# Kernel tuning notes

Measured on AMD Instinct MI355X. Metric: run time of the kernel, lower is better.

Reference implementation:

```python
import jax, jax.numpy as jnp
import numpy as np

B, L, D, H, M = 2, 1024, 1024, 16, 64
DH = D // H  # depth per head


def setup_inputs() -> dict:
    key = jax.random.key(0)
    ks = jax.random.split(key, 7)
    s = 0.02
    return {
        "x": jax.random.normal(ks[0], (B, L, D), jnp.float32),
        "Wq": jax.random.normal(ks[1], (D, D), jnp.float32) * s,
        "Wk": jax.random.normal(ks[2], (D, D), jnp.float32) * s,
        "Wv": jax.random.normal(ks[3], (D, D), jnp.float32) * s,
        "Wo": jax.random.normal(ks[4], (D, D), jnp.float32) * s,
        "rel_k_table": jax.random.normal(ks[5], (2 * M + 1, DH), jnp.float32) * s,
        "rel_v_table": jax.random.normal(ks[6], (2 * M + 1, DH), jnp.float32) * s,
    }


def _rel_idx(length, max_rel):
    # Shaw-style clipped relative position indices: [L, L] in [0, 2*max_rel]
    r = jnp.arange(length)
    return jnp.clip(r[None, :] - r[:, None], -max_rel, max_rel) + max_rel


def _split_heads(t):
    # [B, L, D] -> [B, H, L, DH]
    return t.reshape(B, L, H, DH).transpose(0, 2, 1, 3)


def reference(x, Wq, Wk, Wv, Wo, rel_k_table, rel_v_table):
    q = _split_heads(x @ Wq) * (DH ** -0.5)  # T2T scales q by d_head^-0.5
    k = _split_heads(x @ Wk)
    v = _split_heads(x @ Wv)

    idx = _rel_idx(L, M)
    rel_k = rel_k_table[idx]  # [L, L, DH] gathered keys-relative embeddings
    rel_v = rel_v_table[idx]  # [L, L, DH]

    # _relative_attention_inner(q, k, rel_k, transpose=True)
    logits = jnp.einsum('bhid,bhjd->bhij', q, k) + jnp.einsum('bhid,ijd->bhij', q, rel_k)
    w = jax.nn.softmax(logits, axis=-1)  # [B, H, L, L]; dropout_rate=0 / inference

    # _relative_attention_inner(w, v, rel_v, transpose=False)
    o = jnp.einsum('bhij,bhjd->bhid', w, v) + jnp.einsum('bhij,ijd->bhid', w, rel_v)

    # combine heads then output transform
    o = o.transpose(0, 2, 1, 3).reshape(B, L, D)
    return o @ Wo
```

## Files before the change

### kernel.cpp

```cpp
#include <hip/hip_runtime.h>
#include <hip/hip_bf16.h>
#include <math.h>

#define B_ 2
#define L_ 1024
#define D_ 1024
#define H_ 16
#define DH_ 64
#define M_ 64
#define R_ 129
#define NLD ((size_t)B_ * L_ * D_)
#define DD  ((size_t)D_ * D_)
#define QSCALE 0.18033688011112042f

using bf16x8 = __attribute__((ext_vector_type(8))) short;
using f32x4  = __attribute__((ext_vector_type(4))) float;

__device__ __forceinline__ unsigned short f2bf(float f) {
    unsigned int x = __builtin_bit_cast(unsigned int, f);
    unsigned int r = x + 0x7fffu + ((x >> 16) & 1u);
    return (unsigned short)(r >> 16);
}
__device__ __forceinline__ float bf2f(unsigned short u) {
    unsigned int x = ((unsigned int)u) << 16;
    return __builtin_bit_cast(float, x);
}
__device__ __forceinline__ unsigned int pk2bf(float lo, float hi) {
    __hip_bfloat162 h = __float22bfloat162_rn(float2{lo, hi});
    unsigned int u;
    __builtin_memcpy(&u, &h, 4);
    return u;
}

__global__ __launch_bounds__(256)
void prep(const float* __restrict__ x,
          const float* __restrict__ W0, const float* __restrict__ W1,
          const float* __restrict__ W2, const float* __restrict__ W3,
          const float* __restrict__ relk, const float* __restrict__ relv,
          unsigned short* __restrict__ xb, unsigned short* __restrict__ Wt,
          unsigned short* __restrict__ relkb, unsigned short* __restrict__ relvT)
{
    __shared__ float tile[32][33];
    const int bid = blockIdx.x, t = threadIdx.x;
    if (bid < 2048) {
        const int i = bid * 256 + t;
        float4 v = ((const float4*)x)[i];
        short4 o = { (short)f2bf(v.x), (short)f2bf(v.y), (short)f2bf(v.z), (short)f2bf(v.w) };
        ((short4*)xb)[i] = o;
    } else if (bid < 6144) {
        const int wb = bid - 2048;
        const int z = wb >> 10, rem = wb & 1023;
        const float* W = z == 0 ? W0 : z == 1 ? W1 : z == 2 ? W2 : W3;
        unsigned short* T = Wt + (size_t)z * DD;
        const int k0 = (rem >> 5) * 32, n0 = (rem & 31) * 32;
        const int r = t >> 3, c = (t & 7) * 4;
        float4 v = *(const float4*)&W[(size_t)(k0 + r) * D_ + n0 + c];
        tile[r][c] = v.x; tile[r][c + 1] = v.y; tile[r][c + 2] = v.z; tile[r][c + 3] = v.w;
        __syncthreads();
        short4 o = { (short)f2bf(tile[c][r]),     (short)f2bf(tile[c + 1][r]),
                     (short)f2bf(tile[c + 2][r]), (short)f2bf(tile[c + 3][r]) };
        *(short4*)&T[(size_t)(n0 + r) * D_ + k0 + c] = o;
    } else {
        const int idx = (bid - 6144) * 256 + t;
        if (idx < 144 * 64) {
            const int r = idx >> 6, d = idx & 63;
            relkb[idx] = (r < R_) ? f2bf(relk[r * 64 + d]) : (unsigned short)0;
        }
        if (idx < 64 * 136) {
            const int d = idx / 136, r = idx - d * 136;
            relvT[idx] = (r < R_) ? f2bf(relv[r * 64 + d]) : (unsigned short)0;
        }
    }
}

__global__ __launch_bounds__(256)
void gemm64(const unsigned short* __restrict__ A, const unsigned short* __restrict__ Bt,
            unsigned short* __restrict__ Cb, float* __restrict__ Cf, float scale0)
{
    __shared__ unsigned short As[64][64];
    __shared__ unsigned short Bs[128][64];

    const int t = threadIdx.x, lane = t & 63, wid = t >> 6;
    const int fr = lane & 15, g = lane >> 4;
    const int m0 = blockIdx.y * 64;
    const int nglob = blockIdx.x * 128;
    const int mat = nglob >> 10;
    const int n0 = nglob & 1023;
    const float scale = (mat == 0) ? scale0 : 1.f;
    const int wm = (wid >> 1) * 32, wn = (wid & 1) * 64;

    f32x4 acc[2][4] = {};

    int arow[2], akof[2], adst[2];
#pragma unroll
    for (int c = 0; c < 2; ++c) {
        const int chunk = c * 256 + t;
        arow[c] = chunk >> 3;
        akof[c] = ((chunk & 7) ^ (arow[c] & 7)) * 8;
        adst[c] = chunk * 8;
    }
    int brow[4], bkof[4], bdst[4];
#pragma unroll
    for (int c = 0; c < 4; ++c) {
        const int chunk = c * 256 + t;
        brow[c] = chunk >> 3;
        bkof[c] = ((chunk & 7) ^ (brow[c] & 7)) * 8;
        bdst[c] = chunk * 8;
    }

    const unsigned short* Abase = A  + (size_t)m0 * D_;
    const unsigned short* Bbase = Bt + (size_t)nglob * D_;

    for (int k0 = 0; k0 < D_; k0 += 64) {
        __syncthreads();
#pragma unroll
        for (int c = 0; c < 2; ++c)
            __builtin_amdgcn_global_load_lds(
                (const __attribute__((address_space(1))) void*)(Abase + (size_t)arow[c] * D_ + k0 + akof[c]),
                (__attribute__((address_space(3))) void*)(&As[0][0] + adst[c]), 16, 0, 0);
#pragma unroll
        for (int c = 0; c < 4; ++c)
            __builtin_amdgcn_global_load_lds(
                (const __attribute__((address_space(1))) void*)(Bbase + (size_t)brow[c] * D_ + k0 + bkof[c]),
                (__attribute__((address_space(3))) void*)(&Bs[0][0] + bdst[c]), 16, 0, 0);
        __syncthreads();

#pragma unroll
        for (int kb = 0; kb < 2; ++kb) {
            bf16x8 av[2], bv[4];
#pragma unroll
            for (int i = 0; i < 2; ++i) {
                const int ra = wm + i * 16 + fr;
                av[i] = *(const bf16x8*)&As[ra][(((kb << 2) + g) ^ (ra & 7)) * 8];
            }
#pragma unroll
            for (int j = 0; j < 4; ++j) {
                const int rb = wn + j * 16 + fr;
                bv[j] = *(const bf16x8*)&Bs[rb][(((kb << 2) + g) ^ (rb & 7)) * 8];
            }
#pragma unroll
            for (int i = 0; i < 2; ++i)
#pragma unroll
                for (int j = 0; j < 4; ++j)
                    acc[i][j] = __builtin_amdgcn_mfma_f32_16x16x32_bf16(av[i], bv[j], acc[i][j], 0, 0, 0);
        }
    }

    const int orow = g * 4;
    if (Cb) {
        unsigned short* Cp = Cb + (size_t)mat * NLD;
#pragma unroll
        for (int i = 0; i < 2; ++i)
#pragma unroll
            for (int j = 0; j < 4; ++j) {
                unsigned short* cp = Cp + (size_t)(m0 + wm + i * 16 + orow) * D_ + n0 + wn + j * 16 + fr;
#pragma unroll
                for (int rg = 0; rg < 4; ++rg)
                    cp[(size_t)rg * D_] = f2bf(acc[i][j][rg] * scale);
            }
    } else {
#pragma unroll
        for (int i = 0; i < 2; ++i)
#pragma unroll
            for (int j = 0; j < 4; ++j) {
                float* cp = Cf + (size_t)(m0 + wm + i * 16 + orow) * D_ + n0 + wn + j * 16 + fr;
#pragma unroll
                for (int rg = 0; rg < 4; ++rg)
                    cp[(size_t)rg * D_] = acc[i][j][rg] * scale;
            }
    }
}

__device__ __forceinline__ void stage_k(const unsigned short* src, unsigned short* dst, int t)
{
#pragma unroll
    for (int it = 0; it < 2; ++it) {
        const int c = it * 256 + t;
        const int j = c >> 3;
        const int sc = (c & 7) ^ (j & 7);
        __builtin_amdgcn_global_load_lds(
            (const __attribute__((address_space(1))) void*)(src + (size_t)j * D_ + sc * 8),
            (__attribute__((address_space(3))) void*)(dst + c * 8), 16, 0, 0);
    }
}

__device__ __forceinline__ void write_vt(unsigned short (*Vtl)[64], int jp, int d0, bf16x8 a, bf16x8 b)
{
    const int jlo = (2 * jp) & 7;
    const int jc  = jp >> 2;
#pragma unroll
    for (int e = 0; e < 8; ++e) {
        const int d = d0 + e;
        const unsigned int val = (unsigned int)(unsigned short)a[e]
                               | ((unsigned int)(unsigned short)b[e] << 16);
        *(unsigned int*)&Vtl[d][((jc ^ (d & 7)) << 3) + jlo] = val;
    }
}

__global__ __launch_bounds__(256)
void attn_mfma(const unsigned short* __restrict__ Qb, const unsigned short* __restrict__ Kb,
               const unsigned short* __restrict__ Vb,
               const unsigned short* __restrict__ relkb,
               const unsigned short* __restrict__ relvT,
               const float* __restrict__ relv,
               unsigned short* __restrict__ Ob)
{
    __shared__ unsigned short Klds[2][64][64];
    __shared__ unsigned short Vt[64][64];
    __shared__ unsigned short Plds[64][72];
    __shared__ unsigned short QW[64][136];

    const int t    = threadIdx.x;
    const int lane = t & 63;
    const int w    = t >> 6;
    const int fr   = lane & 15;
    const int g    = lane >> 4;

    const int bx  = blockIdx.x;
    const int xcd = bx & 7, slot = bx >> 3;
    const int bh  = (xcd << 2) | (slot >> 4);
    const int rb  = slot & 15;
    const int b   = bh >> 4, h = bh & 15;
    const int i0  = rb * 64;
    const size_t head = (size_t)b * L_ * D_ + (size_t)h * DH_;

    const int iloc = w * 16 + fr;

    const unsigned short* Kh = Kb + head;
    const unsigned short* Vh = Vb + head;

    stage_k(Kh, &Klds[0][0][0], t);

    const int jp = t & 31, d0v = ((t >> 5) & 7) * 8;
    bf16x8 va  = *(const bf16x8*)(Vh + (size_t)(2 * jp) * D_ + d0v);
    bf16x8 vb2 = *(const bf16x8*)(Vh + (size_t)(2 * jp + 1) * D_ + d0v);

    bf16x8 qf[2];
    {
        const unsigned short* qp = Qb + head + (size_t)(i0 + iloc) * D_;
        qf[0] = *(const bf16x8*)(qp + g * 8);
        qf[1] = *(const bf16x8*)(qp + 32 + g * 8);
    }

#pragma unroll
    for (int rc = 0; rc < 9; ++rc) {
        f32x4 acc = {};
#pragma unroll
        for (int kb = 0; kb < 2; ++kb) {
            bf16x8 rv = *(const bf16x8*)&relkb[(size_t)(rc * 16 + fr) * 64 + kb * 32 + g * 8];
            acc = __builtin_amdgcn_mfma_f32_16x16x32_bf16(rv, qf[kb], acc, 0, 0, 0);
        }
        if (rc < 8) {
            uint2 pk = { pk2bf(acc[0], acc[1]), pk2bf(acc[2], acc[3]) };
            *(uint2*)&QW[iloc][rc * 16 + g * 4] = pk;
        } else if (g == 0) {
            QW[iloc][128] = f2bf(acc[0]);
        }
    }
    if (rb == 0) {
        for (int c = 1 + g; c <= 63 - iloc; c += 4) QW[iloc][c] = 0;
    } else if (rb == 15) {
        for (int c = 128 - iloc + g; c <= 127; c += 4) QW[iloc][c] = 0;
    }

    write_vt(Vt, jp, d0v, va, vb2);
    asm volatile("s_waitcnt vmcnt(0)" ::: "memory");
    __syncthreads();

    const float qr0   = bf2f(QW[iloc][0]);
    const float qr128 = bf2f(QW[iloc][128]);

    f32x4 oacc[4] = {};
    float lpart = 0.f, pe0p = 0.f, pe128p = 0.f;

    int bb = 0;
    for (int jt = 0; jt < 16; ++jt) {
        const bool pre = (jt < 15);
        if (pre) {
            stage_k(Kh + (size_t)(jt + 1) * 64 * D_, &Klds[bb ^ 1][0][0], t);
            const unsigned short* vp = Vh + (size_t)((jt + 1) * 64 + 2 * jp) * D_ + d0v;
            va  = *(const bf16x8*)vp;
            vb2 = *(const bf16x8*)(vp + D_);
        }

        f32x4 s[4];
        __builtin_amdgcn_s_setprio(1);
#pragma unroll
        for (int fc = 0; fc < 4; ++fc) {
            f32x4 a = {};
            const int j = fc * 16 + fr;
#pragma unroll
            for (int kb = 0; kb < 2; ++kb) {
                bf16x8 kv = *(const bf16x8*)&Klds[bb][j][(((kb << 2) + g) ^ (j & 7)) * 8];
                a = __builtin_amdgcn_mfma_f32_16x16x32_bf16(kv, qf[kb], a, 0, 0, 0);
            }
            s[fc] = a;
        }
        __builtin_amdgcn_s_setprio(0);

        bf16x8 vv0[4], vv1[4];
#pragma unroll
        for (int fd = 0; fd < 4; ++fd) {
            const int d = fd * 16 + fr;
            vv0[fd] = *(const bf16x8*)&Vt[d][((g)     ^ (d & 7)) * 8];
            vv1[fd] = *(const bf16x8*)&Vt[d][((4 + g) ^ (d & 7)) * 8];
        }

        const int dt   = (jt - rb) * 64;
        const int relb = dt - iloc + g * 4;

        if (dt <= -128 || dt >= 128) {
            const float qrc = (dt < 0) ? qr0 : qr128;
            float tsum = 0.f;
#pragma unroll
            for (int fc = 0; fc < 4; ++fc) {
                float p0 = exp2f(s[fc][0] + qrc);
                float p1 = exp2f(s[fc][1] + qrc);
                float p2 = exp2f(s[fc][2] + qrc);
                float p3 = exp2f(s[fc][3] + qrc);
                uint2 pk = { pk2bf(p0, p1), pk2bf(p2, p3) };
                *(uint2*)&Plds[iloc][fc * 16 + g * 4] = pk;
                tsum += (p0 + p1) + (p2 + p3);
            }
            lpart += tsum;
            if (dt < 0) pe0p += tsum; else pe128p += tsum;
        } else if (dt == 0) {
#pragma unroll
            for (int fc = 0; fc < 4; ++fc) {
                const int c0 = relb + fc * 16 + M_;
                float pe[4];
#pragma unroll
                for (int reg = 0; reg < 4; ++reg) {
                    pe[reg] = exp2f(s[fc][reg] + bf2f(QW[iloc][c0 + reg]));
                    lpart += pe[reg];
                }
                uint2 pk = { pk2bf(pe[0], pe[1]), pk2bf(pe[2], pe[3]) };
                *(uint2*)&Plds[iloc][fc * 16 + g * 4] = pk;
                QW[iloc][c0 + 0] = (unsigned short)(pk.x & 0xffffu);
                QW[iloc][c0 + 1] = (unsigned short)(pk.x >> 16);
                QW[iloc][c0 + 2] = (unsigned short)(pk.y & 0xffffu);
                QW[iloc][c0 + 3] = (unsigned short)(pk.y >> 16);
            }
        } else {
#pragma unroll
            for (int fc = 0; fc < 4; ++fc) {
                float pe[4];
#pragma unroll
                for (int reg = 0; reg < 4; ++reg) {
                    const int colr = relb + fc * 16 + reg + M_;
                    const int col  = colr < 0 ? 0 : (colr > 128 ? 128 : colr);
                    pe[reg] = exp2f(s[fc][reg] + bf2f(QW[iloc][col]));
                    lpart += pe[reg];
                    if (col == 0)        pe0p   += pe[reg];
                    else if (col == 128) pe128p += pe[reg];
                    else                 QW[iloc][col] = f2bf(pe[reg]);
                }
                uint2 pk = { pk2bf(pe[0], pe[1]), pk2bf(pe[2], pe[3]) };
                *(uint2*)&Plds[iloc][fc * 16 + g * 4] = pk;
            }
        }

        asm volatile("s_waitcnt lgkmcnt(0)" ::: "memory");
        __builtin_amdgcn_sched_barrier(0);

        bf16x8 pa0 = *(const bf16x8*)&Plds[iloc][g * 8];
        bf16x8 pa1 = *(const bf16x8*)&Plds[iloc][32 + g * 8];
        __builtin_amdgcn_s_setprio(1);
#pragma unroll
        for (int fd = 0; fd < 4; ++fd) {
            oacc[fd] = __builtin_amdgcn_mfma_f32_16x16x32_bf16(pa0, vv0[fd], oacc[fd], 0, 0, 0);
            oacc[fd] = __builtin_amdgcn_mfma_f32_16x16x32_bf16(pa1, vv1[fd], oacc[fd], 0, 0, 0);
        }
        __builtin_amdgcn_s_setprio(0);

        if (pre) {
            asm volatile("s_waitcnt lgkmcnt(0)" ::: "memory");
            __builtin_amdgcn_s_barrier();
            write_vt(Vt, jp, d0v, va, vb2);
        }
        asm volatile("s_waitcnt vmcnt(0)" ::: "memory");
        __syncthreads();
        bb ^= 1;
    }

    lpart  += __shfl_xor(lpart, 16);  lpart  += __shfl_xor(lpart, 32);
    pe0p   += __shfl_xor(pe0p, 16);   pe0p   += __shfl_xor(pe0p, 32);
    pe128p += __shfl_xor(pe128p, 16); pe128p += __shfl_xor(pe128p, 32);
    if (g == 0) {
        QW[iloc][0]   = f2bf(pe0p);
        QW[iloc][128] = f2bf(pe128p);
    }
    asm volatile("s_waitcnt lgkmcnt(0)" ::: "memory");
    __builtin_amdgcn_sched_barrier(0);

#pragma unroll
    for (int kc = 0; kc < 4; ++kc) {
        bf16x8 wa = *(const bf16x8*)&QW[iloc][kc * 32 + g * 8];
#pragma unroll
        for (int fd = 0; fd < 4; ++fd) {
            bf16x8 rv = *(const bf16x8*)&relvT[(size_t)(fd * 16 + fr) * 136 + kc * 32 + g * 8];
            oacc[fd] = __builtin_amdgcn_mfma_f32_16x16x32_bf16(wa, rv, oacc[fd], 0, 0, 0);
        }
    }

    float invd[4], pr128[4];
#pragma unroll
    for (int reg = 0; reg < 4; ++reg) {
        const int src = (lane & 48) | (g * 4 + reg);
        invd[reg]  = 1.f / __shfl(lpart, src, 64);
        pr128[reg] = __shfl(pe128p, src, 64);
    }

#pragma unroll
    for (int fd = 0; fd < 4; ++fd) {
        const float r128 = relv[128 * 64 + fd * 16 + fr];
        unsigned short* op = Ob + head + (size_t)(i0 + w * 16 + g * 4) * D_ + fd * 16 + fr;
#pragma unroll
        for (int reg = 0; reg < 4; ++reg)
            op[(size_t)reg * D_] = f2bf((oacc[fd][reg] + pr128[reg] * r128) * invd[reg]);
    }
}

extern "C" void kernel_launch(void* const* d_in, const int* in_sizes, int n_in,
                              void* d_out, int out_size, void* d_ws, size_t ws_size,
                              hipStream_t stream)
{
    const float* x    = (const float*)d_in[0];
    const float* Wq   = (const float*)d_in[1];
    const float* Wk   = (const float*)d_in[2];
    const float* Wv   = (const float*)d_in[3];
    const float* Wo   = (const float*)d_in[4];
    const float* relk = (const float*)d_in[5];
    const float* relv = (const float*)d_in[6];
    float* out = (float*)d_out;

    unsigned short* xb    = (unsigned short*)d_ws;
    unsigned short* Wt    = xb + NLD;
    unsigned short* relkb = Wt + 4 * DD;
    unsigned short* relvT = relkb + 144 * 64;
    unsigned short* QKVb  = relvT + 64 * 136;
    unsigned short* Ob    = QKVb + 3 * NLD;

    prep<<<dim3(6180), 256, 0, stream>>>(x, Wq, Wk, Wv, Wo, relk, relv, xb, Wt, relkb, relvT);

    gemm64<<<dim3(24, 32), 256, 0, stream>>>(xb, Wt, QKVb, nullptr, QSCALE);

    attn_mfma<<<dim3(512), 256, 0, stream>>>(QKVb, QKVb + NLD, QKVb + 2 * NLD,
                                             relkb, relvT, relv, Ob);

    gemm64<<<dim3(8, 32), 256, 0, stream>>>(Ob, Wt + 3 * DD, nullptr, out, 1.f);
}
```

Before: 81.70 us.

## Split attention key tiles across wave pairs with 32-row query blocks

The attention kernel now processes 32 query rows per block instead of 64, and the four waves split into two row groups by two key-column halves. Each wave handles 32 of the 64 keys per tile, and partial softmax sums and output accumulators are reduced through shared memory at the end. The grid doubles to 1024 blocks to raise parallelism and occupancy. In exchange, each block stages the same K/V tiles for half as many rows, so K/V global traffic per output doubles, and the end of the kernel gains extra barriers and a cross-wave reduction.

```diff
diff --git a/kernel.cpp b/kernel.cpp
--- a/kernel.cpp
+++ b/kernel.cpp
@@ -207,24 +207,28 @@
 {
     __shared__ unsigned short Klds[2][64][64];
     __shared__ unsigned short Vt[64][64];
-    __shared__ unsigned short Plds[64][72];
-    __shared__ unsigned short QW[64][136];
+    __shared__ unsigned short Plds[32][88];
+    __shared__ unsigned short QW[32][136];
+    __shared__ float lred[2][32], p0red[2][32], p128red[2][32];
 
     const int t    = threadIdx.x;
     const int lane = t & 63;
     const int w    = t >> 6;
     const int fr   = lane & 15;
     const int g    = lane >> 4;
+    const int wr   = w & 1;
+    const int wj   = w >> 1;
 
     const int bx  = blockIdx.x;
     const int xcd = bx & 7, slot = bx >> 3;
-    const int bh  = (xcd << 2) | (slot >> 4);
-    const int rb  = slot & 15;
+    const int bh  = (xcd << 2) | (slot >> 5);
+    const int rb  = slot & 31;
     const int b   = bh >> 4, h = bh & 15;
-    const int i0  = rb * 64;
+    const int i0  = rb * 32;
     const size_t head = (size_t)b * L_ * D_ + (size_t)h * DH_;
 
-    const int iloc = w * 16 + fr;
+    const int iloc = wr * 16 + fr;
+    const int ig   = i0 + iloc;
 
     const unsigned short* Kh = Kb + head;
     const unsigned short* Vh = Vb + head;
@@ -237,13 +241,12 @@
 
     bf16x8 qf[2];
     {
-        const unsigned short* qp = Qb + head + (size_t)(i0 + iloc) * D_;
+        const unsigned short* qp = Qb + head + (size_t)ig * D_;
         qf[0] = *(const bf16x8*)(qp + g * 8);
         qf[1] = *(const bf16x8*)(qp + 32 + g * 8);
     }
 
-#pragma unroll
-    for (int rc = 0; rc < 9; ++rc) {
+    auto qr_block = [&](int rc) {
         f32x4 acc = {};
 #pragma unroll
         for (int kb = 0; kb < 2; ++kb) {
@@ -256,11 +259,18 @@
         } else if (g == 0) {
             QW[iloc][128] = f2bf(acc[0]);
         }
-    }
-    if (rb == 0) {
-        for (int c = 1 + g; c <= 63 - iloc; c += 4) QW[iloc][c] = 0;
-    } else if (rb == 15) {
-        for (int c = 128 - iloc + g; c <= 127; c += 4) QW[iloc][c] = 0;
+    };
+    if (wj == 0) { qr_block(0); qr_block(1); qr_block(2); qr_block(3); qr_block(8); }
+    else         { qr_block(4); qr_block(5); qr_block(6); qr_block(7); }
+
+    {
+        const int lo_end = 63 - ig;
+        const int hi_beg = 1088 - ig;
+        if (wj == 0) {
+            for (int c = 1 + g; c <= lo_end; c += 4) QW[iloc][c] = 0;
+        } else {
+            for (int c = hi_beg + g; c <= 127; c += 4) QW[iloc][c] = 0;
+        }
     }
 
     write_vt(Vt, jp, d0v, va, vb2);
@@ -283,12 +293,12 @@
             vb2 = *(const bf16x8*)(vp + D_);
         }
 
-        f32x4 s[4];
+        f32x4 s[2];
         __builtin_amdgcn_s_setprio(1);
 #pragma unroll
-        for (int fc = 0; fc < 4; ++fc) {
+        for (int fc = 0; fc < 2; ++fc) {
             f32x4 a = {};
-            const int j = fc * 16 + fr;
+            const int j = wj * 32 + fc * 16 + fr;
 #pragma unroll
             for (int kb = 0; kb < 2; ++kb) {
                 bf16x8 kv = *(const bf16x8*)&Klds[bb][j][(((kb << 2) + g) ^ (j & 7)) * 8];
@@ -298,36 +308,35 @@
         }
         __builtin_amdgcn_s_setprio(0);
 
-        bf16x8 vv0[4], vv1[4];
+        bf16x8 vv[4];
 #pragma unroll
         for (int fd = 0; fd < 4; ++fd) {
             const int d = fd * 16 + fr;
-            vv0[fd] = *(const bf16x8*)&Vt[d][((g)     ^ (d & 7)) * 8];
-            vv1[fd] = *(const bf16x8*)&Vt[d][((4 + g) ^ (d & 7)) * 8];
-        }
-
-        const int dt   = (jt - rb) * 64;
-        const int relb = dt - iloc + g * 4;
-
-        if (dt <= -128 || dt >= 128) {
-            const float qrc = (dt < 0) ? qr0 : qr128;
+            vv[fd] = *(const bf16x8*)&Vt[d][(((wj << 2) + g) ^ (d & 7)) * 8];
+        }
+
+        const int u     = 2 * jt + wj - rb;
+        const int cbase = 32 * u - iloc + g * 4 + 64;
+
+        if (u <= -3 || u >= 3) {
+            const float qrc = (u < 0) ? qr0 : qr128;
             float tsum = 0.f;
 #pragma unroll
-            for (int fc = 0; fc < 4; ++fc) {
+            for (int fc = 0; fc < 2; ++fc) {
                 float p0 = exp2f(s[fc][0] + qrc);
                 float p1 = exp2f(s[fc][1] + qrc);
                 float p2 = exp2f(s[fc][2] + qrc);
                 float p3 = exp2f(s[fc][3] + qrc);
                 uint2 pk = { pk2bf(p0, p1), pk2bf(p2, p3) };
-                *(uint2*)&Plds[iloc][fc * 16 + g * 4] = pk;
+                *(uint2*)&Plds[iloc][wj * 40 + fc * 16 + g * 4] = pk;
                 tsum += (p0 + p1) + (p2 + p3);
             }
             lpart += tsum;
-            if (dt < 0) pe0p += tsum; else pe128p += tsum;
-        } else if (dt == 0) {
-#pragma unroll
-            for (int fc = 0; fc < 4; ++fc) {
-                const int c0 = relb + fc * 16 + M_;
+            if (u < 0) pe0p += tsum; else pe128p += tsum;
+        } else if (u >= -1 && u <= 1) {
+#pragma unroll
+            for (int fc = 0; fc < 2; ++fc) {
+                const int c0 = cbase + fc * 16;
                 float pe[4];
 #pragma unroll
                 for (int reg = 0; reg < 4; ++reg) {
@@ -335,7 +344,7 @@
                     lpart += pe[reg];
                 }
                 uint2 pk = { pk2bf(pe[0], pe[1]), pk2bf(pe[2], pe[3]) };
-                *(uint2*)&Plds[iloc][fc * 16 + g * 4] = pk;
+                *(uint2*)&Plds[iloc][wj * 40 + fc * 16 + g * 4] = pk;
                 QW[iloc][c0 + 0] = (unsigned short)(pk.x & 0xffffu);
                 QW[iloc][c0 + 1] = (unsigned short)(pk.x >> 16);
                 QW[iloc][c0 + 2] = (unsigned short)(pk.y & 0xffffu);
@@ -343,34 +352,33 @@
             }
         } else {
 #pragma unroll
-            for (int fc = 0; fc < 4; ++fc) {
+            for (int fc = 0; fc < 2; ++fc) {
                 float pe[4];
 #pragma unroll
                 for (int reg = 0; reg < 4; ++reg) {
-                    const int colr = relb + fc * 16 + reg + M_;
+                    const int colr = cbase + fc * 16 + reg;
                     const int col  = colr < 0 ? 0 : (colr > 128 ? 128 : colr);
-                    pe[reg] = exp2f(s[fc][reg] + bf2f(QW[iloc][col]));
+                    const float bias = (col == 0) ? qr0 : (col == 128) ? qr128
+                                                        : bf2f(QW[iloc][col]);
+                    pe[reg] = exp2f(s[fc][reg] + bias);
                     lpart += pe[reg];
                     if (col == 0)        pe0p   += pe[reg];
                     else if (col == 128) pe128p += pe[reg];
                     else                 QW[iloc][col] = f2bf(pe[reg]);
                 }
                 uint2 pk = { pk2bf(pe[0], pe[1]), pk2bf(pe[2], pe[3]) };
-                *(uint2*)&Plds[iloc][fc * 16 + g * 4] = pk;
+                *(uint2*)&Plds[iloc][wj * 40 + fc * 16 + g * 4] = pk;
             }
         }
 
         asm volatile("s_waitcnt lgkmcnt(0)" ::: "memory");
         __builtin_amdgcn_sched_barrier(0);
 
-        bf16x8 pa0 = *(const bf16x8*)&Plds[iloc][g * 8];
-        bf16x8 pa1 = *(const bf16x8*)&Plds[iloc][32 + g * 8];
+        bf16x8 pa = *(const bf16x8*)&Plds[iloc][wj * 40 + g * 8];
         __builtin_amdgcn_s_setprio(1);
 #pragma unroll
-        for (int fd = 0; fd < 4; ++fd) {
-            oacc[fd] = __builtin_amdgcn_mfma_f32_16x16x32_bf16(pa0, vv0[fd], oacc[fd], 0, 0, 0);
-            oacc[fd] = __builtin_amdgcn_mfma_f32_16x16x32_bf16(pa1, vv1[fd], oacc[fd], 0, 0, 0);
-        }
+        for (int fd = 0; fd < 4; ++fd)
+            oacc[fd] = __builtin_amdgcn_mfma_f32_16x16x32_bf16(pa, vv[fd], oacc[fd], 0, 0, 0);
         __builtin_amdgcn_s_setprio(0);
 
         if (pre) {
@@ -386,15 +394,25 @@
     lpart  += __shfl_xor(lpart, 16);  lpart  += __shfl_xor(lpart, 32);
     pe0p   += __shfl_xor(pe0p, 16);   pe0p   += __shfl_xor(pe0p, 32);
     pe128p += __shfl_xor(pe128p, 16); pe128p += __shfl_xor(pe128p, 32);
-    if (g == 0) {
-        QW[iloc][0]   = f2bf(pe0p);
-        QW[iloc][128] = f2bf(pe128p);
+    if (lane < 16) {
+        lred[wj][iloc]    = lpart;
+        p0red[wj][iloc]   = pe0p;
+        p128red[wj][iloc] = pe128p;
+    }
+    __syncthreads();
+    const float lt    = lred[0][iloc]    + lred[1][iloc];
+    const float p0t   = p0red[0][iloc]   + p0red[1][iloc];
+    const float p128t = p128red[0][iloc] + p128red[1][iloc];
+    if (wj == 0 && g == 0) {
+        QW[iloc][0]   = f2bf(p0t);
+        QW[iloc][128] = f2bf(p128t);
     }
     asm volatile("s_waitcnt lgkmcnt(0)" ::: "memory");
-    __builtin_amdgcn_sched_barrier(0);
-
-#pragma unroll
-    for (int kc = 0; kc < 4; ++kc) {
+    __syncthreads();
+
+#pragma unroll
+    for (int kk = 0; kk < 2; ++kk) {
+        const int kc = wj * 2 + kk;
         bf16x8 wa = *(const bf16x8*)&QW[iloc][kc * 32 + g * 8];
 #pragma unroll
         for (int fd = 0; fd < 4; ++fd) {
@@ -407,17 +425,32 @@
 #pragma unroll
     for (int reg = 0; reg < 4; ++reg) {
         const int src = (lane & 48) | (g * 4 + reg);
-        invd[reg]  = 1.f / __shfl(lpart, src, 64);
-        pr128[reg] = __shfl(pe128p, src, 64);
-    }
-
-#pragma unroll
-    for (int fd = 0; fd < 4; ++fd) {
-        const float r128 = relv[128 * 64 + fd * 16 + fr];
-        unsigned short* op = Ob + head + (size_t)(i0 + w * 16 + g * 4) * D_ + fd * 16 + fr;
-#pragma unroll
-        for (int reg = 0; reg < 4; ++reg)
-            op[(size_t)reg * D_] = f2bf((oacc[fd][reg] + pr128[reg] * r128) * invd[reg]);
+        invd[reg]  = 1.f / __shfl(lt, src, 64);
+        pr128[reg] = __shfl(p128t, src, 64);
+    }
+
+    float* Of = (float*)&Klds[0][0][0];
+    if (wj == 0) {
+#pragma unroll
+        for (int fd = 0; fd < 4; ++fd)
+#pragma unroll
+            for (int reg = 0; reg < 4; ++reg)
+                Of[(wr * 16 + g * 4 + reg) * 64 + fd * 16 + fr] = oacc[fd][reg];
+    }
+    __syncthreads();
+    if (wj == 1) {
+#pragma unroll
+        for (int fd = 0; fd < 4; ++fd) {
+            const float r128 = relv[128 * 64 + fd * 16 + fr];
+            unsigned short* op = Ob + head + (size_t)(i0 + wr * 16 + g * 4) * D_ + fd * 16 + fr;
+#pragma unroll
+            for (int reg = 0; reg < 4; ++reg) {
+                const float val = oacc[fd][reg]
+                                + Of[(wr * 16 + g * 4 + reg) * 64 + fd * 16 + fr]
+                                + pr128[reg] * r128;
+                op[(size_t)reg * D_] = f2bf(val * invd[reg]);
+            }
+        }
     }
 }
 
@@ -445,8 +478,8 @@
 
     gemm64<<<dim3(24, 32), 256, 0, stream>>>(xb, Wt, QKVb, nullptr, QSCALE);
 
-    attn_mfma<<<dim3(512), 256, 0, stream>>>(QKVb, QKVb + NLD, QKVb + 2 * NLD,
-                                             relkb, relvT, relv, Ob);
+    attn_mfma<<<dim3(1024), 256, 0, stream>>>(QKVb, QKVb + NLD, QKVb + 2 * NLD,
+                                              relkb, relvT, relv, Ob);
 
     gemm64<<<dim3(8, 32), 256, 0, stream>>>(Ob, Wt + 3 * DD, nullptr, out, 1.f);
 }
```

New measurement: 82.70 us. About the same (+1.2%).

## Triple-buffer K tiles and double-buffer V to deepen prefetch pipeline

Applied to the files above, without the earlier changes.

K tiles are prefetched two iterations ahead into a three-slot LDS ring and V^T is double-buffered, so each iteration drops one barrier and waits only on the older loads through partial vmcnt counts. V loads are issued as inline-asm global loads so the counter accounting is predictable. The clamped relative-bias read at columns 0 and 128 now uses register copies instead of LDS. This relies on stage_k issuing exactly two global loads per thread, uses more LDS (which may lower occupancy), and is fragile if the compiler reorders memory operations.

```diff
diff --git a/kernel.cpp b/kernel.cpp
--- a/kernel.cpp
+++ b/kernel.cpp
@@ -205,8 +205,8 @@
                const float* __restrict__ relv,
                unsigned short* __restrict__ Ob)
 {
-    __shared__ unsigned short Klds[2][64][64];
-    __shared__ unsigned short Vt[64][64];
+    __shared__ unsigned short Klds[3][64][64];
+    __shared__ unsigned short Vt[2][64][64];
     __shared__ unsigned short Plds[64][72];
     __shared__ unsigned short QW[64][136];
 
@@ -230,10 +230,15 @@
     const unsigned short* Vh = Vb + head;
 
     stage_k(Kh, &Klds[0][0][0], t);
+    stage_k(Kh + (size_t)64 * D_, &Klds[1][0][0], t);
 
     const int jp = t & 31, d0v = ((t >> 5) & 7) * 8;
-    bf16x8 va  = *(const bf16x8*)(Vh + (size_t)(2 * jp) * D_ + d0v);
-    bf16x8 vb2 = *(const bf16x8*)(Vh + (size_t)(2 * jp + 1) * D_ + d0v);
+    bf16x8 va, vb2;
+    {
+        const unsigned short* vsrc = Vh + (size_t)(2 * jp) * D_ + d0v;
+        asm volatile("global_load_dwordx4 %0, %1, off" : "=v"(va)  : "v"(vsrc)      : "memory");
+        asm volatile("global_load_dwordx4 %0, %1, off" : "=v"(vb2) : "v"(vsrc + D_) : "memory");
+    }
 
     bf16x8 qf[2];
     {
@@ -263,8 +268,9 @@
         for (int c = 128 - iloc + g; c <= 127; c += 4) QW[iloc][c] = 0;
     }
 
-    write_vt(Vt, jp, d0v, va, vb2);
     asm volatile("s_waitcnt vmcnt(0)" ::: "memory");
+    __builtin_amdgcn_sched_barrier(0);
+    write_vt(Vt[0], jp, d0v, va, vb2);
     __syncthreads();
 
     const float qr0   = bf2f(QW[iloc][0]);
@@ -273,14 +279,16 @@
     f32x4 oacc[4] = {};
     float lpart = 0.f, pe0p = 0.f, pe128p = 0.f;
 
-    int bb = 0;
+    int kcur = 0;
     for (int jt = 0; jt < 16; ++jt) {
-        const bool pre = (jt < 15);
-        if (pre) {
-            stage_k(Kh + (size_t)(jt + 1) * 64 * D_, &Klds[bb ^ 1][0][0], t);
-            const unsigned short* vp = Vh + (size_t)((jt + 1) * 64 + 2 * jp) * D_ + d0v;
-            va  = *(const bf16x8*)vp;
-            vb2 = *(const bf16x8*)(vp + D_);
+        if (jt < 15) {
+            const unsigned short* vsrc = Vh + (size_t)((jt + 1) * 64 + 2 * jp) * D_ + d0v;
+            asm volatile("global_load_dwordx4 %0, %1, off" : "=v"(va)  : "v"(vsrc)      : "memory");
+            asm volatile("global_load_dwordx4 %0, %1, off" : "=v"(vb2) : "v"(vsrc + D_) : "memory");
+        }
+        if (jt < 14) {
+            int kpre = kcur + 2; if (kpre >= 3) kpre -= 3;
+            stage_k(Kh + (size_t)(jt + 2) * 64 * D_, &Klds[kpre][0][0], t);
         }
 
         f32x4 s[4];
@@ -291,7 +299,7 @@
             const int j = fc * 16 + fr;
 #pragma unroll
             for (int kb = 0; kb < 2; ++kb) {
-                bf16x8 kv = *(const bf16x8*)&Klds[bb][j][(((kb << 2) + g) ^ (j & 7)) * 8];
+                bf16x8 kv = *(const bf16x8*)&Klds[kcur][j][(((kb << 2) + g) ^ (j & 7)) * 8];
                 a = __builtin_amdgcn_mfma_f32_16x16x32_bf16(kv, qf[kb], a, 0, 0, 0);
             }
             s[fc] = a;
@@ -302,8 +310,8 @@
 #pragma unroll
         for (int fd = 0; fd < 4; ++fd) {
             const int d = fd * 16 + fr;
-            vv0[fd] = *(const bf16x8*)&Vt[d][((g)     ^ (d & 7)) * 8];
-            vv1[fd] = *(const bf16x8*)&Vt[d][((4 + g) ^ (d & 7)) * 8];
+            vv0[fd] = *(const bf16x8*)&Vt[jt & 1][d][((g)     ^ (d & 7)) * 8];
+            vv1[fd] = *(const bf16x8*)&Vt[jt & 1][d][((4 + g) ^ (d & 7)) * 8];
         }
 
         const int dt   = (jt - rb) * 64;
@@ -349,7 +357,9 @@
                 for (int reg = 0; reg < 4; ++reg) {
                     const int colr = relb + fc * 16 + reg + M_;
                     const int col  = colr < 0 ? 0 : (colr > 128 ? 128 : colr);
-                    pe[reg] = exp2f(s[fc][reg] + bf2f(QW[iloc][col]));
+                    const float bias = (col == 0) ? qr0 : (col == 128) ? qr128
+                                                        : bf2f(QW[iloc][col]);
+                    pe[reg] = exp2f(s[fc][reg] + bias);
                     lpart += pe[reg];
                     if (col == 0)        pe0p   += pe[reg];
                     else if (col == 128) pe128p += pe[reg];
@@ -373,14 +383,15 @@
         }
         __builtin_amdgcn_s_setprio(0);
 
-        if (pre) {
-            asm volatile("s_waitcnt lgkmcnt(0)" ::: "memory");
-            __builtin_amdgcn_s_barrier();
-            write_vt(Vt, jp, d0v, va, vb2);
-        }
-        asm volatile("s_waitcnt vmcnt(0)" ::: "memory");
-        __syncthreads();
-        bb ^= 1;
+        if (jt < 15) {
+            if (jt < 14) asm volatile("s_waitcnt vmcnt(2)" ::: "memory");
+            else         asm volatile("s_waitcnt vmcnt(0)" ::: "memory");
+            __builtin_amdgcn_sched_barrier(0);
+            write_vt(Vt[(jt + 1) & 1], jp, d0v, va, vb2);
+        }
+        asm volatile("s_waitcnt lgkmcnt(0)" ::: "memory");
+        __builtin_amdgcn_s_barrier();
+        kcur = (kcur == 2) ? 0 : kcur + 1;
     }
 
     lpart  += __shfl_xor(lpart, 16);  lpart  += __shfl_xor(lpart, 32);
```

Result: slower. 84.07 us (+2.9%).
